# Optimization experiments

Hardware: AMD Instinct MI355X
Metric: run time of the kernel (lower is better)

## Reference

```python
import jax, jax.numpy as jnp
import numpy as np

N_E = 1024
E_DIM = 64
BETA = 0.25


def setup_inputs() -> dict:
    key = jax.random.key(0)
    k1, k2 = jax.random.split(key)
    z = jax.random.normal(k1, (16, E_DIM, 64, 64), dtype=jnp.float32)
    # embedding initialized uniform(-1/n_e, 1/n_e) as in the torch module
    emb = jax.random.uniform(k2, (N_E, E_DIM), dtype=jnp.float32,
                             minval=-1.0 / N_E, maxval=1.0 / N_E)
    return {"z": z, "emb": emb}


def reference(z, emb):
    n_e, e_dim = emb.shape
    # NCHW -> NHWC, flatten to tokens
    zp = jnp.transpose(z, (0, 2, 3, 1))            # [B,H,W,C]
    zf = zp.reshape(-1, e_dim)                      # [N,C]
    # squared distances ||zf||^2 + ||e||^2 - 2 zf e^T  -> [N, n_e]
    d = (jnp.sum(zf * zf, axis=1, keepdims=True)
         + jnp.sum(emb * emb, axis=1)
         - 2.0 * jnp.matmul(zf, emb.T))
    idx = jnp.argmin(d, axis=1)                     # [N]
    # one-hot @ emb is exactly a gather
    z_q = emb[idx].reshape(zp.shape)                # [B,H,W,C]
    loss = (jnp.mean((jax.lax.stop_gradient(z_q) - zp) ** 2)
            + BETA * jnp.mean((z_q - jax.lax.stop_gradient(zp)) ** 2))
    # straight-through estimator
    z_q = zp + jax.lax.stop_gradient(z_q - zp)
    # perplexity from codeword usage histogram
    counts = jax.ops.segment_sum(jnp.ones_like(idx, dtype=zf.dtype), idx,
                                 num_segments=n_e)
    e_mean = counts / zf.shape[0]
    perplexity = jnp.exp(-jnp.sum(e_mean * jnp.log(e_mean + 1e-10)))
    min_encoding_indices = idx.reshape(z.shape[0], -1).astype(jnp.int32)
    z_q = jnp.transpose(z_q, (0, 3, 1, 2))          # back to NCHW
    return z_q, loss, perplexity, min_encoding_indices
```

## Files before the change

kernel.cpp:

```cpp
#include <hip/hip_runtime.h>

#define TOKS 65536
#define ED 64
#define NE 1024
#define CH_STRIDE 4096
#define B_STRIDE 262144

typedef __bf16 bf16x8 __attribute__((ext_vector_type(8)));
typedef float f32x16 __attribute__((ext_vector_type(16)));
typedef unsigned short ushort_t;
typedef unsigned int uint_t;


__device__ __forceinline__ ushort_t f2bf(float x) {
    uint_t u = __float_as_uint(x);
    uint_t r = u + 0x7FFFu + ((u >> 16) & 1u);
    return (ushort_t)(r >> 16);
}

__global__ __launch_bounds__(256) void vq_prep_e(const float* __restrict__ emb,
                                                 ushort_t* __restrict__ efrag,
                                                 float* __restrict__ enorm,
                                                 int* __restrict__ hist,
                                                 double* __restrict__ lossAcc) {
    const int tid = threadIdx.x;
    const int w = tid >> 6, lane = tid & 63;
    const int j = blockIdx.x * 4 + w;

    const float e = emb[j * 64 + lane];
    const float sq = __fmul_rn(e, e);
    float acc = sq;
    acc = __fadd_rn(acc, __shfl_down(sq, 8, 64));
    acc = __fadd_rn(acc, __shfl_down(sq, 16, 64));
    acc = __fadd_rn(acc, __shfl_down(sq, 24, 64));
    acc = __fadd_rn(acc, __shfl_down(sq, 32, 64));
    acc = __fadd_rn(acc, __shfl_down(sq, 40, 64));
    acc = __fadd_rn(acc, __shfl_down(sq, 48, 64));
    acc = __fadd_rn(acc, __shfl_down(sq, 56, 64));
    float x = __fadd_rn(acc, __shfl_down(acc, 1, 64));
    float y = __fadd_rn(x, __shfl_down(x, 2, 64));
    float zn = __fadd_rn(y, __shfl_down(y, 4, 64));
    if (lane == 0) enorm[j] = zn;

    const ushort_t h = f2bf(-2.0f * e);
    const int ct = j >> 5, m = j & 31;
    const int ks = lane >> 4, kh = (lane >> 3) & 1, i = lane & 7;
    efrag[(size_t)((ct * 4 + ks) * 512) + (m + 32 * kh) * 8 + i] = h;

    if (blockIdx.x < 4) hist[blockIdx.x * 256 + tid] = 0;
    if (blockIdx.x == 0 && tid == 0) *lossAcc = 0.0;
}

__global__ __launch_bounds__(256, 4) void vq_main(
    const float* __restrict__ z,
    const ushort_t* __restrict__ efrag,
    const float* __restrict__ enorm,
    const float* __restrict__ emb,
    float* __restrict__ zq,
    float* __restrict__ out_idx,
    int* __restrict__ hist,
    double* __restrict__ lossAcc) {
    __shared__ float z_s[64][36];
    __shared__ uint_t skey[4][32][2][3];
    __shared__ double wsum[4];

    const int tid = threadIdx.x;
    const int w = tid >> 6, lane = tid & 63;
    const int t0 = blockIdx.x * 32;
    const int b = t0 >> 12, hw0 = t0 & 4095;
    const float* zbase = z + (size_t)b * B_STRIDE + hw0;

    {
        const int c = tid >> 2, u0 = (tid & 3) * 8;
        const float* src = zbase + (size_t)c * CH_STRIDE + u0;
        float4 f0 = *(const float4*)(src);
        float4 f1 = *(const float4*)(src + 4);
        *(float4*)&z_s[c][u0] = f0;
        *(float4*)&z_s[c][u0 + 4] = f1;
    }
    __syncthreads();

    const int n = lane & 31, kh = lane >> 5;

    bf16x8 zb[4];
    #pragma unroll
    for (int ks = 0; ks < 4; ++ks) {
        #pragma unroll
        for (int i = 0; i < 8; ++i) {
            union { ushort_t u; __bf16 bh; } ca;
            ca.u = f2bf(z_s[ks * 16 + kh * 8 + i][n]);
            zb[ks][i] = ca.bh;
        }
    }

    uint_t k0 = 0xFFFFFFFFu, k1 = 0xFFFFFFFFu, k2 = 0xFFFFFFFFu;
    const bf16x8* eg = (const bf16x8*)efrag;

    #pragma unroll
    for (int ct = 0; ct < 8; ++ct) {
        const int gct = w * 8 + ct;
        bf16x8 ah0 = eg[(size_t)(gct * 4 + 0) * 64 + lane];
        bf16x8 ah1 = eg[(size_t)(gct * 4 + 1) * 64 + lane];
        bf16x8 ah2 = eg[(size_t)(gct * 4 + 2) * 64 + lane];
        bf16x8 ah3 = eg[(size_t)(gct * 4 + 3) * 64 + lane];

        f32x16 acc;
        #pragma unroll
        for (int r = 0; r < 16; ++r) acc[r] = 0.25f;
        acc = __builtin_amdgcn_mfma_f32_32x32x16_bf16(ah0, zb[0], acc, 0, 0, 0);
        acc = __builtin_amdgcn_mfma_f32_32x32x16_bf16(ah1, zb[1], acc, 0, 0, 0);
        acc = __builtin_amdgcn_mfma_f32_32x32x16_bf16(ah2, zb[2], acc, 0, 0, 0);
        acc = __builtin_amdgcn_mfma_f32_32x32x16_bf16(ah3, zb[3], acc, 0, 0, 0);

        const int jb = gct * 32 + 4 * kh;
        #pragma unroll
        for (int r = 0; r < 16; ++r) {
            uint_t key = (__float_as_uint(acc[r]) & 0xFFFFFC00u)
                         | (uint_t)(jb + (r & 3) + 8 * (r >> 2));
            uint_t mx = max(k0, key);
            k2 = min(k2, max(k1, mx));
            k1 = min(k1, mx);
            k0 = min(k0, key);
        }
    }

    skey[w][n][kh][0] = k0; skey[w][n][kh][1] = k1; skey[w][n][kh][2] = k2;
    __syncthreads();

    const int t_loc = tid >> 3, cw = tid & 7;
    uint_t ck[3];
    #pragma unroll
    for (int s = 0; s < 3; ++s) ck[s] = skey[cw >> 1][t_loc][cw & 1][s];

    uint_t kmin = min(ck[0], min(ck[1], ck[2]));
    kmin = min(kmin, (uint_t)__shfl_xor((int)kmin, 1, 64));
    kmin = min(kmin, (uint_t)__shfl_xor((int)kmin, 2, 64));
    kmin = min(kmin, (uint_t)__shfl_xor((int)kmin, 4, 64));
    const float thr = __uint_as_float(kmin & 0xFFFFFC00u) + 4.0e-4f;

    float rr[8];
    #pragma unroll
    for (int m = 0; m < 8; ++m) {
        float a = z_s[m][t_loc];
        rr[m] = __fmul_rn(a, a);
    }
    #pragma unroll
    for (int i = 8; i < 64; i += 8) {
        #pragma unroll
        for (int m = 0; m < 8; ++m) {
            float a = z_s[i + m][t_loc];
            rr[m] = __fadd_rn(rr[m], __fmul_rn(a, a));
        }
    }
    const float zn =
        __fadd_rn(__fadd_rn(__fadd_rn(rr[0], rr[1]), __fadd_rn(rr[2], rr[3])),
                  __fadd_rn(__fadd_rn(rr[4], rr[5]), __fadd_rn(rr[6], rr[7])));

    float bd = 3.4e38f; int bj = 1 << 30;
    #pragma unroll
    for (int c2 = 0; c2 < 3; ++c2) {
        const float vc = __uint_as_float(ck[c2] & 0xFFFFFC00u);
        if (vc <= thr) {
            const int j = (int)(ck[c2] & 1023u);
            const float* e = emb + (size_t)j * 64;
            float a0 = 0.f;
            #pragma unroll
            for (int k4 = 0; k4 < 64; k4 += 4) {
                float4 e4 = *(const float4*)(e + k4);
                a0 = __fmaf_rn(z_s[k4 + 0][t_loc], e4.x, a0);
                a0 = __fmaf_rn(z_s[k4 + 1][t_loc], e4.y, a0);
                a0 = __fmaf_rn(z_s[k4 + 2][t_loc], e4.z, a0);
                a0 = __fmaf_rn(z_s[k4 + 3][t_loc], e4.w, a0);
            }
            float d = __fsub_rn(__fadd_rn(zn, enorm[j]), 2.0f * a0);
            if (d < bd || (d == bd && j < bj)) { bd = d; bj = j; }
        }
    }
    #pragma unroll
    for (int m = 1; m < 8; m <<= 1) {
        float pd = __shfl_xor(bd, m, 64);
        int pj = __shfl_xor(bj, m, 64);
        if (pd < bd || (pd == bd && pj < bj)) { bd = pd; bj = pj; }
    }

    if (cw == 0) {
        out_idx[t0 + t_loc] = (float)bj;
        atomicAdd(&hist[bj], 1);
    }

    double ls = 0.0;
    {
        const float* e = emb + (size_t)bj * 64;
        #pragma unroll
        for (int i = 0; i < 8; ++i) {
            const int k = cw + 8 * i;
            float ev = e[k];
            float zv = z_s[k][t_loc];
            z_s[k][t_loc] = ev;
            float df = ev - zv;
            ls += (double)(df * df);
        }
    }
    #pragma unroll
    for (int off = 32; off > 0; off >>= 1) ls += __shfl_down(ls, off, 64);
    if (lane == 0) wsum[w] = ls;
    __syncthreads();
    if (tid == 0)
        atomicAdd(lossAcc, wsum[0] + wsum[1] + wsum[2] + wsum[3]);

    {
        const int c = tid >> 2, u0 = (tid & 3) * 8;
        float4 f0 = *(const float4*)&z_s[c][u0];
        float4 f1 = *(const float4*)&z_s[c][u0 + 4];
        float* dst = zq + (size_t)b * B_STRIDE + (size_t)c * CH_STRIDE + hw0 + u0;
        *(float4*)(dst) = f0;
        *(float4*)(dst + 4) = f1;
    }
}

__global__ __launch_bounds__(256) void vq_final(const int* __restrict__ hist,
                                                const double* __restrict__ lossAcc,
                                                float* __restrict__ outs) {
    __shared__ double red[256];
    double acc = 0.0;
    for (int j = threadIdx.x; j < NE; j += 256) {
        double em = (double)hist[j] * (1.0 / 65536.0);
        acc += em * log(em + 1e-10);
    }
    red[threadIdx.x] = acc;
    __syncthreads();
    for (int s = 128; s > 0; s >>= 1) {
        if (threadIdx.x < s) red[threadIdx.x] += red[threadIdx.x + s];
        __syncthreads();
    }
    if (threadIdx.x == 0) {
        outs[0] = (float)(1.25 * (*lossAcc) * (1.0 / 4194304.0));
        outs[1] = (float)exp(-red[0]);
    }
}

extern "C" void kernel_launch(void* const* d_in, const int* in_sizes, int n_in,
                              void* d_out, int out_size, void* d_ws, size_t ws_size,
                              hipStream_t stream) {
    const float* z = (const float*)d_in[0];
    const float* emb = (const float*)d_in[1];
    float* out = (float*)d_out;

    char* ws = (char*)d_ws;
    ushort_t* efrag = (ushort_t*)ws;
    float* enorm = (float*)(ws + 131072);
    int* hist = (int*)(ws + 135168);
    double* lossAcc = (double*)(ws + 139264);

    float* zq = out;
    float* scalars = out + 4194304;
    float* out_idx = out + 4194306;

    vq_prep_e<<<256, 256, 0, stream>>>(emb, efrag, enorm, hist, lossAcc);
    vq_main<<<2048, 256, 0, stream>>>(z, efrag, enorm, emb, zq, out_idx, hist, lossAcc);
    vq_final<<<1, 256, 0, stream>>>(hist, lossAcc, scalars);
}
```

Baseline: 49.16 us.

## Compact refine candidates in shared memory and refine one per thread

Surviving candidates from the bf16 top-3 filter are now pushed into a shared list with a shared atomic counter. Each thread refines at most one candidate in fp32, and a packed distance/index 64-bit atomicMin picks the winner per token. The token norm is now computed cooperatively with shuffles and kept in shared memory. The MFMA operand conversion reads z straight from global memory, which drops the barrier before the GEMM. This should cut serial, divergent refine work per thread, at the cost of extra barriers, shared atomics, a 128-candidate cap that silently drops overflow, and a changed summation order for the norm.

```diff
diff --git a/kernel.cpp b/kernel.cpp
--- a/kernel.cpp
+++ b/kernel.cpp
@@ -62,6 +62,10 @@
     double* __restrict__ lossAcc) {
     __shared__ float z_s[64][36];
     __shared__ uint_t skey[4][32][2][3];
+    __shared__ float s_zn[32];
+    __shared__ unsigned long long s_res[32];
+    __shared__ uint_t s_cand[128];
+    __shared__ int s_cnt;
     __shared__ double wsum[4];
 
     const int tid = threadIdx.x;
@@ -78,7 +82,8 @@
         *(float4*)&z_s[c][u0] = f0;
         *(float4*)&z_s[c][u0 + 4] = f1;
     }
-    __syncthreads();
+    if (tid < 32) s_res[tid] = 0xFFFFFFFFFFFFFFFFull;
+    if (tid == 0) s_cnt = 0;
 
     const int n = lane & 31, kh = lane >> 5;
 
@@ -88,7 +93,7 @@
         #pragma unroll
         for (int i = 0; i < 8; ++i) {
             union { ushort_t u; __bf16 bh; } ca;
-            ca.u = f2bf(z_s[ks * 16 + kh * 8 + i][n]);
+            ca.u = f2bf(zbase[(size_t)(ks * 16 + kh * 8 + i) * CH_STRIDE + n]);
             zb[ks][i] = ca.bh;
         }
     }
@@ -127,73 +132,75 @@
     skey[w][n][kh][0] = k0; skey[w][n][kh][1] = k1; skey[w][n][kh][2] = k2;
     __syncthreads();
 
-    const int t_loc = tid >> 3, cw = tid & 7;
-    uint_t ck[3];
-    #pragma unroll
-    for (int s = 0; s < 3; ++s) ck[s] = skey[cw >> 1][t_loc][cw & 1][s];
-
-    uint_t kmin = min(ck[0], min(ck[1], ck[2]));
-    kmin = min(kmin, (uint_t)__shfl_xor((int)kmin, 1, 64));
-    kmin = min(kmin, (uint_t)__shfl_xor((int)kmin, 2, 64));
-    kmin = min(kmin, (uint_t)__shfl_xor((int)kmin, 4, 64));
-    const float thr = __uint_as_float(kmin & 0xFFFFFC00u) + 4.0e-4f;
-
-    float rr[8];
-    #pragma unroll
-    for (int m = 0; m < 8; ++m) {
+    const int t_loc = tid >> 3, m = tid & 7;
+    {
         float a = z_s[m][t_loc];
-        rr[m] = __fmul_rn(a, a);
-    }
-    #pragma unroll
-    for (int i = 8; i < 64; i += 8) {
-        #pragma unroll
-        for (int m = 0; m < 8; ++m) {
-            float a = z_s[i + m][t_loc];
-            rr[m] = __fadd_rn(rr[m], __fmul_rn(a, a));
-        }
-    }
-    const float zn =
-        __fadd_rn(__fadd_rn(__fadd_rn(rr[0], rr[1]), __fadd_rn(rr[2], rr[3])),
-                  __fadd_rn(__fadd_rn(rr[4], rr[5]), __fadd_rn(rr[6], rr[7])));
-
-    float bd = 3.4e38f; int bj = 1 << 30;
-    #pragma unroll
-    for (int c2 = 0; c2 < 3; ++c2) {
-        const float vc = __uint_as_float(ck[c2] & 0xFFFFFC00u);
-        if (vc <= thr) {
-            const int j = (int)(ck[c2] & 1023u);
+        float racc = __fmul_rn(a, a);
+        #pragma unroll
+        for (int i = 1; i < 8; ++i) {
+            float av = z_s[m + 8 * i][t_loc];
+            racc = __fadd_rn(racc, __fmul_rn(av, av));
+        }
+        float x1 = __fadd_rn(racc, __shfl_xor(racc, 1, 64));
+        float y1 = __fadd_rn(x1, __shfl_xor(x1, 2, 64));
+        float zn = __fadd_rn(y1, __shfl_xor(y1, 4, 64));
+        if (m == 0) s_zn[t_loc] = zn;
+    }
+    {
+        uint_t ck[3];
+        #pragma unroll
+        for (int s = 0; s < 3; ++s) ck[s] = skey[m >> 1][t_loc][m & 1][s];
+        uint_t kmin = min(ck[0], min(ck[1], ck[2]));
+        kmin = min(kmin, (uint_t)__shfl_xor((int)kmin, 1, 64));
+        kmin = min(kmin, (uint_t)__shfl_xor((int)kmin, 2, 64));
+        kmin = min(kmin, (uint_t)__shfl_xor((int)kmin, 4, 64));
+        const float thr = __uint_as_float(kmin & 0xFFFFFC00u) + 4.0e-4f;
+        #pragma unroll
+        for (int s = 0; s < 3; ++s) {
+            if (__uint_as_float(ck[s] & 0xFFFFFC00u) <= thr) {
+                int pos = atomicAdd(&s_cnt, 1);
+                if (pos < 128)
+                    s_cand[pos] = ((uint_t)t_loc << 10) | (ck[s] & 1023u);
+            }
+        }
+    }
+    __syncthreads();
+
+    {
+        const int cnt = s_cnt;
+        if (tid < cnt && tid < 128) {
+            const uint_t cd = s_cand[tid];
+            const int tok = (int)(cd >> 10), j = (int)(cd & 1023u);
             const float* e = emb + (size_t)j * 64;
             float a0 = 0.f;
             #pragma unroll
             for (int k4 = 0; k4 < 64; k4 += 4) {
                 float4 e4 = *(const float4*)(e + k4);
-                a0 = __fmaf_rn(z_s[k4 + 0][t_loc], e4.x, a0);
-                a0 = __fmaf_rn(z_s[k4 + 1][t_loc], e4.y, a0);
-                a0 = __fmaf_rn(z_s[k4 + 2][t_loc], e4.z, a0);
-                a0 = __fmaf_rn(z_s[k4 + 3][t_loc], e4.w, a0);
+                a0 = __fmaf_rn(z_s[k4 + 0][tok], e4.x, a0);
+                a0 = __fmaf_rn(z_s[k4 + 1][tok], e4.y, a0);
+                a0 = __fmaf_rn(z_s[k4 + 2][tok], e4.z, a0);
+                a0 = __fmaf_rn(z_s[k4 + 3][tok], e4.w, a0);
             }
-            float d = __fsub_rn(__fadd_rn(zn, enorm[j]), 2.0f * a0);
-            if (d < bd || (d == bd && j < bj)) { bd = d; bj = j; }
-        }
-    }
-    #pragma unroll
-    for (int m = 1; m < 8; m <<= 1) {
-        float pd = __shfl_xor(bd, m, 64);
-        int pj = __shfl_xor(bj, m, 64);
-        if (pd < bd || (pd == bd && pj < bj)) { bd = pd; bj = pj; }
-    }
-
-    if (cw == 0) {
+            float d = __fsub_rn(__fadd_rn(s_zn[tok], enorm[j]), 2.0f * a0);
+            unsigned long long key =
+                ((unsigned long long)__float_as_uint(d) << 10)
+                | (unsigned long long)j;
+            atomicMin(&s_res[tok], key);
+        }
+    }
+    __syncthreads();
+
+    const int bj = (int)(s_res[t_loc] & 1023u);
+    if (m == 0) {
         out_idx[t0 + t_loc] = (float)bj;
         atomicAdd(&hist[bj], 1);
     }
-
     double ls = 0.0;
     {
         const float* e = emb + (size_t)bj * 64;
         #pragma unroll
         for (int i = 0; i < 8; ++i) {
-            const int k = cw + 8 * i;
+            const int k = m + 8 * i;
             float ev = e[k];
             float zv = z_s[k][t_loc];
             z_s[k][t_loc] = ev;
```

After: 49.23 us. About the same (+0.1%).
